# Kernel tuning notes

Measured on AMD Instinct MI355X. Metric: run time of the kernel, lower is better.

Reference implementation:

```python
import jax, jax.numpy as jnp
import numpy as np

EMB = 1024
N_HEADS = 16
HEAD = EMB // N_HEADS
EPS = 1e-5


def layernorm(x, g, b):
    mu = jnp.mean(x, axis=-1, keepdims=True)
    var = jnp.var(x, axis=-1, keepdims=True)
    return (x - mu) * jax.lax.rsqrt(var + EPS) * g + b


def setup_inputs() -> dict:
    key = jax.random.key(0)
    ks = jax.random.split(key, 12)
    s = lambda fan_in: 1.0 / np.sqrt(fan_in)
    return {
        "x": jax.random.normal(ks[0], (8, 1024, EMB), dtype=jnp.float32),
        "ln1_g": jnp.ones((EMB,), jnp.float32),
        "ln1_b": jnp.zeros((EMB,), jnp.float32),
        "wq": jax.random.uniform(ks[1], (EMB, EMB), jnp.float32, -s(EMB), s(EMB)),
        "wk": jax.random.uniform(ks[2], (EMB, EMB), jnp.float32, -s(EMB), s(EMB)),
        "wv": jax.random.uniform(ks[3], (EMB, EMB), jnp.float32, -s(EMB), s(EMB)),
        "w_proj": jax.random.uniform(ks[4], (EMB, EMB), jnp.float32, -s(EMB), s(EMB)),
        "b_proj": jnp.zeros((EMB,), jnp.float32),
        "ln2_g": jnp.ones((EMB,), jnp.float32),
        "ln2_b": jnp.zeros((EMB,), jnp.float32),
        "w1": jax.random.uniform(ks[5], (EMB, 4 * EMB), jnp.float32, -s(EMB), s(EMB)),
        "b1": jnp.zeros((4 * EMB,), jnp.float32),
        "w2": jax.random.uniform(ks[6], (4 * EMB, EMB), jnp.float32, -s(4 * EMB), s(4 * EMB)),
        "b2": jnp.zeros((EMB,), jnp.float32),
    }


def reference(x, ln1_g, ln1_b, wq, wk, wv, w_proj, b_proj, ln2_g, ln2_b, w1, b1, w2, b2):
    B, T, E = x.shape
    h = layernorm(x, ln1_g, ln1_b)
    # per-head no-bias projections == one big matmul then split into heads
    q = (h @ wq).reshape(B, T, N_HEADS, HEAD).transpose(0, 2, 1, 3)  # [B,H,T,D]
    k = (h @ wk).reshape(B, T, N_HEADS, HEAD).transpose(0, 2, 1, 3)
    v = (h @ wv).reshape(B, T, N_HEADS, HEAD).transpose(0, 2, 1, 3)
    scores = jnp.einsum("bhqd,bhkd->bhqk", q, k) * (HEAD ** -0.5)
    causal = jnp.tril(jnp.ones((T, T), dtype=bool))
    scores = jnp.where(causal, scores, -jnp.inf)
    wei = jax.nn.softmax(scores, axis=-1)  # dropout is identity at eval
    attn = jnp.einsum("bhqk,bhkd->bhqd", wei, v)
    attn = attn.transpose(0, 2, 1, 3).reshape(B, T, E)
    out = x + attn @ w_proj + b_proj
    h2 = layernorm(out, ln2_g, ln2_b)
    mlp = jax.nn.gelu(h2 @ w1 + b1, approximate=False) @ w2 + b2
    return out + mlp
```

## Files before the change

kernel.cpp:

```cpp
#include <hip/hip_runtime.h>
#include <hip/hip_bf16.h>

#define EMB 1024
#define NH 16
#define HD 64
#define BATCH 8
#define SEQ 1024
#define ROWS (BATCH*SEQ)

typedef unsigned short ushort_t;
typedef __attribute__((ext_vector_type(8))) short bf16x8;
typedef __attribute__((ext_vector_type(4))) float f32x4;
typedef __attribute__((ext_vector_type(16))) float f32x16;

__device__ __forceinline__ float bf2f(ushort_t u){
    union { unsigned int i; float f; } v; v.i = ((unsigned int)u) << 16; return v.f;
}
__device__ __forceinline__ ushort_t f2bf(float f){
    unsigned int u = __float_as_uint(f);
    unsigned int r = (u + 0x7FFFu + ((u >> 16) & 1u)) >> 16;
    return (ushort_t)r;
}
__device__ __forceinline__ void gload16(const ushort_t* g, ushort_t* l){
    __builtin_amdgcn_global_load_lds(
        (const __attribute__((address_space(1))) void*)g,
        (__attribute__((address_space(3))) void*)l,
        16, 0, 0);
}
__device__ __forceinline__ float gelu_f(float v){
    float x = fabsf(v) * 0.70710678118654752f;
    float t = __builtin_amdgcn_rcpf(1.0f + 0.3275911f * x);
    float poly = t*(0.254829592f + t*(-0.284496736f + t*(1.421413741f + t*(-1.453152027f + t*1.061405429f))));
    float erfa = 1.0f - poly * __expf(-x*x);
    float erfv = (v >= 0.f) ? erfa : -erfa;
    return 0.5f * v * (1.0f + erfv);
}

__global__ __launch_bounds__(256) void prep_kernel(const float* __restrict__ x,
                                                   const float* __restrict__ ln1_g,
                                                   const float* __restrict__ ln1_b,
                                                   ushort_t* __restrict__ h1,
                                                   const float* __restrict__ wq,
                                                   const float* __restrict__ wk,
                                                   const float* __restrict__ wv,
                                                   const float* __restrict__ w_proj,
                                                   const float* __restrict__ w1,
                                                   const float* __restrict__ w2,
                                                   ushort_t* __restrict__ wqkv_t,
                                                   ushort_t* __restrict__ wproj_t,
                                                   ushort_t* __restrict__ w1_t,
                                                   ushort_t* __restrict__ w2_t){
    int bid = blockIdx.x;
    int tid = threadIdx.x;
    if (bid < ROWS){
        __shared__ float ss[4], qq[4];
        __shared__ float mu_s, sc_s;
        const float* xr = x + (size_t)bid * EMB;
        float4 f = *(const float4*)(xr + tid*4);
        float v[4] = {f.x, f.y, f.z, f.w};
        float s = v[0]+v[1]+v[2]+v[3];
        float q = v[0]*v[0]+v[1]*v[1]+v[2]*v[2]+v[3]*v[3];
        #pragma unroll
        for (int o = 32; o > 0; o >>= 1){ s += __shfl_down(s, o); q += __shfl_down(q, o); }
        int wave = tid >> 6, lane = tid & 63;
        if (lane == 0){ ss[wave] = s; qq[wave] = q; }
        __syncthreads();
        if (tid == 0){
            float S = ss[0]+ss[1]+ss[2]+ss[3];
            float Q = qq[0]+qq[1]+qq[2]+qq[3];
            float mu = S * (1.0f/EMB);
            float var = Q * (1.0f/EMB) - mu*mu;
            mu_s = mu; sc_s = rsqrtf(var + 1e-5f);
        }
        __syncthreads();
        float mu = mu_s, sc = sc_s;
        float4 gu = *(const float4*)(ln1_g + tid*4);
        float4 bu = *(const float4*)(ln1_b + tid*4);
        ushort4 o4;
        o4.x = f2bf((v[0]-mu)*sc*gu.x + bu.x);
        o4.y = f2bf((v[1]-mu)*sc*gu.y + bu.y);
        o4.z = f2bf((v[2]-mu)*sc*gu.z + bu.z);
        o4.w = f2bf((v[3]-mu)*sc*gu.w + bu.w);
        *(ushort4*)(h1 + (size_t)bid*EMB + tid*4) = o4;
    } else {
        __shared__ ushort_t t[32][33];
        int j = bid - ROWS;
        const float* in; ushort_t* out; int K, N, bx, by;
        if (j < 3072){
            int which = j >> 10, jj = j & 1023;
            in = (which == 0) ? wq : (which == 1) ? wk : wv;
            out = wqkv_t + (size_t)which * 1024 * 1024;
            K = 1024; N = 1024; bx = jj & 31; by = jj >> 5;
        } else if (j < 4096){
            int jj = j - 3072;
            in = w_proj; out = wproj_t; K = 1024; N = 1024; bx = jj & 31; by = jj >> 5;
        } else if (j < 8192){
            int jj = j - 4096;
            in = w1; out = w1_t; K = 1024; N = 4096; bx = jj & 127; by = jj >> 7;
        } else {
            int jj = j - 8192;
            in = w2; out = w2_t; K = 4096; N = 1024; bx = jj & 31; by = jj >> 5;
        }
        int tx = tid & 31, ty = tid >> 5;
        #pragma unroll
        for (int r = 0; r < 4; ++r)
            t[ty + r*8][tx] = f2bf(in[(size_t)(by*32 + ty + r*8) * N + bx*32 + tx]);
        __syncthreads();
        #pragma unroll
        for (int r = 0; r < 4; ++r)
            out[(size_t)(bx*32 + ty + r*8) * K + by*32 + tx] = t[tx][ty + r*8];
    }
}

__global__ __launch_bounds__(256) void ln_kernel(const float* __restrict__ xin,
                                                 const float* __restrict__ g,
                                                 const float* __restrict__ bia,
                                                 ushort_t* __restrict__ out){
    int row = blockIdx.x;
    int tid = threadIdx.x;
    const float* x = xin + (size_t)row * EMB;
    float4 f = *(const float4*)(x + tid*4);
    float v[4] = {f.x, f.y, f.z, f.w};
    float s = v[0]+v[1]+v[2]+v[3];
    float q = v[0]*v[0]+v[1]*v[1]+v[2]*v[2]+v[3]*v[3];
    #pragma unroll
    for (int o = 32; o > 0; o >>= 1){ s += __shfl_down(s, o); q += __shfl_down(q, o); }
    __shared__ float ss[4], qq[4];
    __shared__ float mu_s, sc_s;
    int wave = tid >> 6, lane = tid & 63;
    if (lane == 0){ ss[wave] = s; qq[wave] = q; }
    __syncthreads();
    if (tid == 0){
        float S = ss[0]+ss[1]+ss[2]+ss[3];
        float Q = qq[0]+qq[1]+qq[2]+qq[3];
        float mu = S * (1.0f/EMB);
        float var = Q * (1.0f/EMB) - mu*mu;
        mu_s = mu; sc_s = rsqrtf(var + 1e-5f);
    }
    __syncthreads();
    float mu = mu_s, sc = sc_s;
    float4 gu = *(const float4*)(g + tid*4);
    float4 bu = *(const float4*)(bia + tid*4);
    ushort4 o4;
    o4.x = f2bf((v[0]-mu)*sc*gu.x + bu.x);
    o4.y = f2bf((v[1]-mu)*sc*gu.y + bu.y);
    o4.z = f2bf((v[2]-mu)*sc*gu.z + bu.z);
    o4.w = f2bf((v[3]-mu)*sc*gu.w + bu.w);
    *(ushort4*)(out + (size_t)row*EMB + tid*4) = o4;
}

template<int MODE>
__global__ __launch_bounds__(512, 6) void gemm_kernel(const ushort_t* __restrict__ A,
                                                      const ushort_t* __restrict__ Bt,
                                                      const float* __restrict__ bias,
                                                      const float* __restrict__ resid,
                                                      void* __restrict__ out,
                                                      int M, int N, int K){
    __shared__ ushort_t As[128*64];
    __shared__ ushort_t Bs[128*64];
    int tid = threadIdx.x;
    int lane = tid & 63, wave = tid >> 6;
    int l31 = lane & 31, half = lane >> 5;
    int wm = wave >> 1, wn = wave & 1;
    int bid = blockIdx.x;
    int m0 = (bid & 63) * 128, n0 = (bid >> 6) * 128;

    f32x16 acc[2];
    #pragma unroll
    for (int j=0;j<2;j++)
        #pragma unroll
        for (int r=0;r<16;r++) acc[j][r] = 0.f;

    int lr  = lane >> 3;
    int lch = lane & 7;
    const ushort_t* gA = A  + (size_t)(m0 + wave*16 + lr)*K + (lch ^ lr)*8;
    const ushort_t* gB = Bt + (size_t)(n0 + wave*16 + lr)*K + (lch ^ lr)*8;
    ushort_t* lA = &As[(wave*16)*64];
    ushort_t* lB = &Bs[(wave*16)*64];
    int sx = lane & 7;

    for (int k0 = 0; k0 < K; k0 += 64){
        gload16(gA + k0, lA);
        gload16(gA + (size_t)8*K + k0, lA + 8*64);
        gload16(gB + k0, lB);
        gload16(gB + (size_t)8*K + k0, lB + 8*64);
        __syncthreads();
        #pragma unroll
        for (int s = 0; s < 4; ++s){
            int ch = ((s<<1) | half) ^ sx;
            bf16x8 af = *(const bf16x8*)&As[(wm*32 + l31)*64 + ch*8];
            bf16x8 bfr[2];
            #pragma unroll
            for (int j=0;j<2;j++) bfr[j] = *(const bf16x8*)&Bs[(wn*64 + j*32 + l31)*64 + ch*8];
            #pragma unroll
            for (int j=0;j<2;j++)
                acc[j] = __builtin_amdgcn_mfma_f32_32x32x16_bf16(af, bfr[j], acc[j], 0,0,0);
        }
        __syncthreads();
    }

    int rowoff = 4*half;
    #pragma unroll
    for (int j=0;j<2;j++){
        int n = n0 + wn*64 + j*32 + l31;
        #pragma unroll
        for (int reg=0; reg<16; ++reg){
            int m = m0 + wm*32 + (reg&3) + 8*(reg>>2) + rowoff;
            float v = acc[j][reg];
            size_t idx = (size_t)m*N + n;
            if (MODE == 0){
                ((ushort_t*)out)[idx] = f2bf(v);
            } else if (MODE == 1){
                v += bias[n] + resid[idx];
                ((float*)out)[idx] = v;
            } else if (MODE == 2){
                v += bias[n];
                ((ushort_t*)out)[idx] = f2bf(gelu_f(v));
            } else {
                v += bias[n] + resid[idx];
                ((float*)out)[idx] = v;
            }
        }
    }
}

__global__ __launch_bounds__(256) void attn_kernel(const ushort_t* __restrict__ qkv,
                                                   ushort_t* __restrict__ attn_out){
    __shared__ ushort_t Qs[128*64];
    __shared__ ushort_t Ks[64*64];
    __shared__ ushort_t Vts[64][72];
    __shared__ ushort_t Ps[128*64];

    int tid = threadIdx.x;
    int lane = tid & 63, wave = tid >> 6;
    int quad = lane >> 4, l15 = lane & 15;
    int pair = blockIdx.x;
    int bh = blockIdx.y;
    int b = bh >> 4, h = bh & 15;
    size_t tb = (size_t)b * SEQ;

    int lr = lane >> 3, lch = lane & 7;
    int tr = tid >> 3;
    int tc = (tid & 7) * 8;
    int sw_w = tid & 7;
    int sx = l15 & 7;

    for (int t = 0; t < 2; ++t){
        int qi = t ? (7 - pair) : pair;

        {
            const ushort_t* gq = qkv + (size_t)(tb + qi*128 + wave*32 + lr)*3072 + h*64 + (lch^lr)*8;
            ushort_t* lq = &Qs[(wave*32)*64];
            #pragma unroll
            for (int p = 0; p < 4; ++p)
                gload16(gq + (size_t)(p*8)*3072, lq + p*8*64);
        }

        f32x4 o_acc[4][2];
        #pragma unroll
        for (int i=0;i<4;i++)
            #pragma unroll
            for (int j=0;j<2;j++) o_acc[i][j] = (f32x4){0.f,0.f,0.f,0.f};
        float m_st[2] = {-1e30f, -1e30f};
        float l_st[2] = {0.f, 0.f};

        int nj = 2*qi + 2;
        for (int j = 0; j < nj; ++j){
            {
                const ushort_t* gk = qkv + (size_t)(tb + j*64 + wave*16 + lr)*3072 + 1024 + h*64 + (lch^lr)*8;
                ushort_t* lk = &Ks[(wave*16)*64];
                gload16(gk, lk);
                gload16(gk + (size_t)8*3072, lk + 8*64);
            }
            #pragma unroll
            for (int p = 0; p < 2; ++p){
                int r = tr + p*32;
                bf16x8 vv = *(const bf16x8*)(qkv + (size_t)(tb + j*64 + r)*3072 + 2048 + h*64 + tc);
                int kcol = r ^ (sw_w << 3);
                #pragma unroll
                for (int c = 0; c < 8; ++c) Vts[tc + c][kcol] = (ushort_t)vv[c];
            }
            __syncthreads();

            f32x4 st[4][2];
            #pragma unroll
            for (int mt=0;mt<4;mt++)
                #pragma unroll
                for (int nt=0;nt<2;nt++) st[mt][nt] = (f32x4){0.f,0.f,0.f,0.f};
            #pragma unroll
            for (int kf = 0; kf < 2; ++kf){
                int ch = (kf*4 + quad) ^ sx;
                bf16x8 ak[4], bq[2];
                #pragma unroll
                for (int mt=0;mt<4;mt++) ak[mt] = *(const bf16x8*)&Ks[(mt*16 + l15)*64 + ch*8];
                #pragma unroll
                for (int nt=0;nt<2;nt++) bq[nt] = *(const bf16x8*)&Qs[(wave*32 + nt*16 + l15)*64 + ch*8];
                #pragma unroll
                for (int mt=0;mt<4;mt++)
                    #pragma unroll
                    for (int nt=0;nt<2;nt++)
                        st[mt][nt] = __builtin_amdgcn_mfma_f32_16x16x32_bf16(ak[mt], bq[nt], st[mt][nt], 0,0,0);
            }

            bool need_mask = (j >= 2*qi);
            #pragma unroll
            for (int mt=0;mt<4;mt++)
                #pragma unroll
                for (int nt=0;nt<2;nt++)
                    #pragma unroll
                    for (int r=0;r<4;r++){
                        float s = st[mt][nt][r] * 0.125f;
                        if (need_mask){
                            int kg = j*64 + mt*16 + quad*4 + r;
                            int qg = qi*128 + wave*32 + nt*16 + l15;
                            if (kg > qg) s = -1e30f;
                        }
                        st[mt][nt][r] = s;
                    }

            #pragma unroll
            for (int nt = 0; nt < 2; ++nt){
                float mx = st[0][nt][0];
                #pragma unroll
                for (int mt=0;mt<4;mt++)
                    #pragma unroll
                    for (int r=0;r<4;r++) mx = fmaxf(mx, st[mt][nt][r]);
                mx = fmaxf(mx, __shfl_xor(mx, 16));
                mx = fmaxf(mx, __shfl_xor(mx, 32));
                float mnew = fmaxf(m_st[nt], mx);
                float al = __expf(m_st[nt] - mnew);
                float ps = 0.f;
                #pragma unroll
                for (int mt=0;mt<4;mt++)
                    #pragma unroll
                    for (int r=0;r<4;r++){
                        float p = __expf(st[mt][nt][r] - mnew);
                        st[mt][nt][r] = p;
                        ps += p;
                    }
                ps += __shfl_xor(ps, 16);
                ps += __shfl_xor(ps, 32);
                l_st[nt] = l_st[nt]*al + ps;
                m_st[nt] = mnew;
                #pragma unroll
                for (int mtd=0;mtd<4;mtd++)
                    #pragma unroll
                    for (int r=0;r<4;r++) o_acc[mtd][nt][r] *= al;
                #pragma unroll
                for (int mt=0;mt<4;mt++){
                    int slot = (mt*2 + (quad>>1)) ^ sx;
                    ushort4 pk;
                    pk.x = f2bf(st[mt][nt][0]); pk.y = f2bf(st[mt][nt][1]);
                    pk.z = f2bf(st[mt][nt][2]); pk.w = f2bf(st[mt][nt][3]);
                    *(ushort4*)&Ps[(wave*32 + nt*16 + l15)*64 + slot*8 + (quad&1)*4] = pk;
                }
            }

            #pragma unroll
            for (int kf = 0; kf < 2; ++kf){
                bf16x8 av[4], bp[2];
                #pragma unroll
                for (int mtd=0;mtd<4;mtd++){
                    int d = mtd*16 + l15;
                    int col = (kf*32 + quad*8) ^ (((d >> 3) & 7) << 3);
                    av[mtd] = *(const bf16x8*)&Vts[d][col];
                }
                #pragma unroll
                for (int nt=0;nt<2;nt++){
                    int ch = (kf*4 + quad) ^ sx;
                    bp[nt] = *(const bf16x8*)&Ps[(wave*32 + nt*16 + l15)*64 + ch*8];
                }
                #pragma unroll
                for (int mtd=0;mtd<4;mtd++)
                    #pragma unroll
                    for (int nt=0;nt<2;nt++)
                        o_acc[mtd][nt] = __builtin_amdgcn_mfma_f32_16x16x32_bf16(av[mtd], bp[nt], o_acc[mtd][nt], 0,0,0);
            }
            __syncthreads();
        }

        #pragma unroll
        for (int nt = 0; nt < 2; ++nt){
            float inv = 1.0f / l_st[nt];
            size_t tok = tb + qi*128 + wave*32 + nt*16 + l15;
            #pragma unroll
            for (int mtd = 0; mtd < 4; ++mtd){
                ushort4 ok;
                ok.x = f2bf(o_acc[mtd][nt][0]*inv); ok.y = f2bf(o_acc[mtd][nt][1]*inv);
                ok.z = f2bf(o_acc[mtd][nt][2]*inv); ok.w = f2bf(o_acc[mtd][nt][3]*inv);
                *(ushort4*)(attn_out + tok*EMB + h*64 + mtd*16 + quad*4) = ok;
            }
        }
    }
}

extern "C" void kernel_launch(void* const* d_in, const int* in_sizes, int n_in,
                              void* d_out, int out_size, void* d_ws, size_t ws_size,
                              hipStream_t stream){
    const float* x      = (const float*)d_in[0];
    const float* ln1_g  = (const float*)d_in[1];
    const float* ln1_b  = (const float*)d_in[2];
    const float* wq     = (const float*)d_in[3];
    const float* wk     = (const float*)d_in[4];
    const float* wv     = (const float*)d_in[5];
    const float* w_proj = (const float*)d_in[6];
    const float* b_proj = (const float*)d_in[7];
    const float* ln2_g  = (const float*)d_in[8];
    const float* ln2_b  = (const float*)d_in[9];
    const float* w1     = (const float*)d_in[10];
    const float* b1     = (const float*)d_in[11];
    const float* w2     = (const float*)d_in[12];
    const float* b2     = (const float*)d_in[13];
    float* outp = (float*)d_out;

    char* ws = (char*)d_ws;
    size_t off = 0;
    auto alloc = [&](size_t bytes)->char*{ char* p = ws + off; off += (bytes + 255) & ~255ULL; return p; };
    ushort_t* wqkv_t = (ushort_t*)alloc((size_t)3072*1024*2);
    ushort_t* wproj_t= (ushort_t*)alloc((size_t)1024*1024*2);
    ushort_t* w1_t   = (ushort_t*)alloc((size_t)4096*1024*2);
    ushort_t* w2_t   = (ushort_t*)alloc((size_t)1024*4096*2);
    ushort_t* qkv    = (ushort_t*)alloc((size_t)ROWS*3072*2);
    ushort_t* hbuf   = (ushort_t*)alloc((size_t)ROWS*1024*2);
    float*    out32  = (float*)  alloc((size_t)ROWS*1024*4);
    ushort_t* mid    = (ushort_t*)alloc((size_t)ROWS*4096*2);
    ushort_t* h1 = hbuf;
    ushort_t* attn = hbuf;
    ushort_t* h2 = qkv;

    dim3 blk(256);
    dim3 gblk(512);
    prep_kernel<<<dim3(20480), blk, 0, stream>>>(x, ln1_g, ln1_b, h1,
                                                 wq, wk, wv, w_proj, w1, w2,
                                                 wqkv_t, wproj_t, w1_t, w2_t);
    gemm_kernel<0><<<dim3(64*(3072/128)), gblk, 0, stream>>>(h1, wqkv_t, nullptr, nullptr, qkv, ROWS, 3072, 1024);
    attn_kernel<<<dim3(4,128), blk, 0, stream>>>(qkv, attn);
    gemm_kernel<1><<<dim3(64*(1024/128)), gblk, 0, stream>>>(attn, wproj_t, b_proj, x, out32, ROWS, 1024, 1024);
    ln_kernel<<<ROWS, blk, 0, stream>>>(out32, ln2_g, ln2_b, h2);
    gemm_kernel<2><<<dim3(64*(4096/128)), gblk, 0, stream>>>(h2, w1_t, b1, nullptr, mid, ROWS, 4096, 1024);
    gemm_kernel<3><<<dim3(64*(1024/128)), gblk, 0, stream>>>(mid, w2_t, b2, out32, outp, ROWS, 1024, 4096);
}
```

Baseline: 489.9 us.

## Double-buffer GEMM LDS tiles to overlap global loads with MFMA compute

Gives the GEMM kernel two LDS buffers and prefetches the next K tile with global_load_lds while MFMAs run on the current one. Manual vmcnt waits and raw s_barrier calls replace __syncthreads. This hides global load latency behind compute, at the cost of doubling LDS per block (64KB) and lowering the launch-bounds occupancy hint from 6 to 4. The loop assumes NT is even.

```diff
diff --git a/kernel.cpp b/kernel.cpp
--- a/kernel.cpp
+++ b/kernel.cpp
@@ -150,14 +150,14 @@
 }
 
 template<int MODE>
-__global__ __launch_bounds__(512, 6) void gemm_kernel(const ushort_t* __restrict__ A,
+__global__ __launch_bounds__(512, 4) void gemm_kernel(const ushort_t* __restrict__ A,
                                                       const ushort_t* __restrict__ Bt,
                                                       const float* __restrict__ bias,
                                                       const float* __restrict__ resid,
                                                       void* __restrict__ out,
                                                       int M, int N, int K){
-    __shared__ ushort_t As[128*64];
-    __shared__ ushort_t Bs[128*64];
+    __shared__ ushort_t As[2][128*64];
+    __shared__ ushort_t Bs[2][128*64];
     int tid = threadIdx.x;
     int lane = tid & 63, wave = tid >> 6;
     int l31 = lane & 31, half = lane >> 5;
@@ -175,29 +175,48 @@
     int lch = lane & 7;
     const ushort_t* gA = A  + (size_t)(m0 + wave*16 + lr)*K + (lch ^ lr)*8;
     const ushort_t* gB = Bt + (size_t)(n0 + wave*16 + lr)*K + (lch ^ lr)*8;
-    ushort_t* lA = &As[(wave*16)*64];
-    ushort_t* lB = &Bs[(wave*16)*64];
+    int lo = (wave*16)*64;
     int sx = lane & 7;
-
-    for (int k0 = 0; k0 < K; k0 += 64){
-        gload16(gA + k0, lA);
-        gload16(gA + (size_t)8*K + k0, lA + 8*64);
-        gload16(gB + k0, lB);
-        gload16(gB + (size_t)8*K + k0, lB + 8*64);
-        __syncthreads();
-        #pragma unroll
-        for (int s = 0; s < 4; ++s){
-            int ch = ((s<<1) | half) ^ sx;
-            bf16x8 af = *(const bf16x8*)&As[(wm*32 + l31)*64 + ch*8];
-            bf16x8 bfr[2];
-            #pragma unroll
-            for (int j=0;j<2;j++) bfr[j] = *(const bf16x8*)&Bs[(wn*64 + j*32 + l31)*64 + ch*8];
-            #pragma unroll
-            for (int j=0;j<2;j++)
-                acc[j] = __builtin_amdgcn_mfma_f32_32x32x16_bf16(af, bfr[j], acc[j], 0,0,0);
-        }
-        __syncthreads();
-    }
+    int NT = K >> 6;
+
+#define GTILE(B, T)                                                                       \
+    {                                                                                     \
+        if ((T) + 1 < NT){                                                                \
+            int nk0 = ((T) + 1) << 6;                                                     \
+            gload16(gA + nk0,               &As[(B)^1][lo]);                              \
+            gload16(gA + (size_t)8*K + nk0, &As[(B)^1][lo + 8*64]);                       \
+            gload16(gB + nk0,               &Bs[(B)^1][lo]);                              \
+            gload16(gB + (size_t)8*K + nk0, &Bs[(B)^1][lo + 8*64]);                       \
+            asm volatile("s_waitcnt vmcnt(4)" ::: "memory");                              \
+        } else {                                                                          \
+            asm volatile("s_waitcnt vmcnt(0)" ::: "memory");                              \
+        }                                                                                 \
+        __builtin_amdgcn_s_barrier();                                                     \
+        asm volatile("" ::: "memory");                                                    \
+        _Pragma("unroll")                                                                 \
+        for (int s = 0; s < 4; ++s){                                                      \
+            int ch = ((s<<1) | half) ^ sx;                                                \
+            bf16x8 af  = *(const bf16x8*)&As[B][(wm*32 + l31)*64 + ch*8];                 \
+            bf16x8 bf0 = *(const bf16x8*)&Bs[B][(wn*64 + l31)*64 + ch*8];                 \
+            bf16x8 bf1 = *(const bf16x8*)&Bs[B][(wn*64 + 32 + l31)*64 + ch*8];            \
+            acc[0] = __builtin_amdgcn_mfma_f32_32x32x16_bf16(af, bf0, acc[0], 0,0,0);     \
+            acc[1] = __builtin_amdgcn_mfma_f32_32x32x16_bf16(af, bf1, acc[1], 0,0,0);     \
+        }                                                                                 \
+        asm volatile("" ::: "memory");                                                    \
+        __builtin_amdgcn_s_barrier();                                                     \
+        asm volatile("" ::: "memory");                                                    \
+    }
+
+    gload16(gA,               &As[0][lo]);
+    gload16(gA + (size_t)8*K, &As[0][lo + 8*64]);
+    gload16(gB,               &Bs[0][lo]);
+    gload16(gB + (size_t)8*K, &Bs[0][lo + 8*64]);
+
+    for (int t = 0; t < NT; t += 2){
+        GTILE(0, t)
+        GTILE(1, t+1)
+    }
+#undef GTILE
 
     int rowoff = 4*half;
     #pragma unroll
```

Result: faster. 458.3 us (-6.5%).
